# Kernel tuning notes

Measured on AMD Instinct MI355X. Metric: run time of the kernel, lower is better.

Reference implementation:

```python
import jax, jax.numpy as jnp
import numpy as np

B = 4096          # walker batch
S0, S1 = 8, 8     # up / down spins
N = S0 + S1       # total electrons
M = 4             # nucleons
D = 16            # determinants
N_ONE = [256, 256, 256, 256]
N_TWO = [32, 32, 32, 32]


def setup_inputs() -> dict:
    key = jax.random.key(0)
    ks = jax.random.split(key, 16)
    f0 = 8 + 3 * 4 * M              # 56, first-layer one-stream input
    f1 = 3 * N_ONE[0] + 2 * N_TWO[0]  # 832, later-layer one-stream input
    s = 0.05
    return {
        "x": jax.random.normal(ks[0], (B, N, 3), jnp.float32),
        "nucleon_pos": jnp.asarray([[0.0, 0.0, 0.0], [0.0, 0.0, 1.4],
                                    [1.2, 0.0, 0.0], [0.0, 1.2, 0.7]], jnp.float32),
        "v0_w": s * jax.random.normal(ks[1], (N_ONE[0], f0), jnp.float32),
        "v0_b": s * jax.random.normal(ks[2], (N_ONE[0],), jnp.float32),
        "v_w": s * jax.random.normal(ks[3], (3, N_ONE[0], f1), jnp.float32),
        "v_b": s * jax.random.normal(ks[4], (3, N_ONE[0]), jnp.float32),
        "w0_w": s * jax.random.normal(ks[5], (N_TWO[0], 4), jnp.float32),
        "w0_b": s * jax.random.normal(ks[6], (N_TWO[0],), jnp.float32),
        "w_w": s * jax.random.normal(ks[7], (3, N_TWO[0], N_TWO[0]), jnp.float32),
        "w_b": s * jax.random.normal(ks[8], (3, N_TWO[0]), jnp.float32),
        "env_w": s * jax.random.normal(ks[9], (D, N, N_ONE[-1]), jnp.float32),
        "env_g": jax.random.uniform(ks[10], (D, N), jnp.float32),
        "sigma": jax.random.uniform(ks[11], (D, N, M), jnp.float32),
        "pi": jax.random.uniform(ks[12], (D, N, M), jnp.float32),
    }


def _safe_norm(v, axis):
    # ||v||_2 with a zero (not NaN) gradient at v == 0 (diagonal e-e distances).
    s = jnp.sum(v * v, axis=axis)
    return jnp.sqrt(jnp.where(s == 0, 1.0, s)) * (s > 0)


def reference(x, nucleon_pos, v0_w, v0_b, v_w, v_b, w0_w, w0_b, w_w, w_b,
              env_w, env_g, sigma, pi):
    b = x.shape[0]
    # electron-electron stream: [B,N,N,4], [b,i,j] = x_j - x_i, |x_j - x_i|
    tev = x[:, None, :, :] - x[:, :, None, :]
    two = jnp.concatenate([tev, _safe_norm(tev, -1)[..., None]], axis=-1)
    # electron-nucleus: oev[b,m,n] = x_n - R_m  -> [B,M,N,3]
    oev = x[:, None, :, :] - nucleon_pos[:, None, :]
    oed = jnp.linalg.norm(oev, axis=-1)                     # [B,M,N]
    one = jnp.concatenate([oev, oed[..., None]], axis=-1)   # [B,M,N,4]
    one = jnp.transpose(one, (0, 2, 1, 3)).reshape(b, N, 4 * M)  # [B,N,4M]
    oev_p = jnp.transpose(oev, (0, 2, 1, 3))                # [B,N,M,3]

    for l in range(len(N_ONE)):
        g1u = jnp.mean(one[:, :S0], axis=1)                 # [B,F]
        g1d = jnp.mean(one[:, S0:], axis=1)
        g2u = jnp.mean(two[:, :, :S0, :], axis=2)           # [B,N,F2]
        g2d = jnp.mean(two[:, :, S0:, :], axis=2)
        f = jnp.concatenate([
            one,
            jnp.broadcast_to(g1u[:, None], (b, N, g1u.shape[-1])),
            jnp.broadcast_to(g1d[:, None], (b, N, g1d.shape[-1])),
            g2u, g2d], axis=-1)
        Wv, bv = (v0_w, v0_b) if l == 0 else (v_w[l - 1], v_b[l - 1])
        Ww, bw = (w0_w, w0_b) if l == 0 else (w_w[l - 1], w_b[l - 1])
        new_one = jnp.tanh(jnp.einsum('bnf,of->bno', f, Wv) + bv)
        new_two = jnp.tanh(jnp.einsum('bijf,of->bijo', two, Ww) + bw)
        if l > 0 and N_ONE[l] == N_ONE[l - 1] and N_TWO[l] == N_TWO[l - 1]:
            new_one = new_one + one
            new_two = new_two + two
        one, two = new_one, new_two

    r = jnp.linalg.norm(oev_p, axis=-1)                     # [B,N,M]
    F = N_ONE[-1]

    def block(rows, cols):
        ew = env_w[:, rows]                # [D,ni,F]
        eg = env_g[:, rows]                # [D,ni]
        sg = jnp.abs(sigma[:, rows])       # [D,ni,M]
        pw = pi[:, rows]                   # [D,ni,M]
        h = one[:, cols]                   # [B,nj,F]
        rj = r[:, cols]                    # [B,nj,M]
        # sum_f (w*h + g) = w.h + F*g
        lin = jnp.einsum('kif,bjf->bkij', ew, h) + F * eg[None, :, :, None]
        env = jnp.zeros(lin.shape, lin.dtype)
        for m in range(M):                 # small static loop over nucleons
            env = env + pw[None, :, :, None, m] * jnp.exp(
                -sg[None, :, :, None, m] * rj[:, None, None, :, m])
        return lin * env                   # [B,D,ni,nj]

    psi_up = block(slice(0, S0), slice(0, S0))
    psi_dn = block(slice(0, S1), slice(S0, N))  # original reuses row params k*N+i
    d = jnp.linalg.det(psi_up) * jnp.linalg.det(psi_dn)     # [B,D]
    return jnp.sum(d, axis=1)                               # [B]
```

## Files before the change

kernel.cpp:

```cpp
#include <hip/hip_runtime.h>
#include <cmath>

namespace {

typedef unsigned short u16;
typedef unsigned int u32;
using short8  = __attribute__((ext_vector_type(8))) short;
using float4v = __attribute__((ext_vector_type(4))) float;

constexpr size_t MB_HI   = 0;
constexpr size_t MB_LO   = 638976;
constexpr size_t L0_HI   = 1277952;
constexpr size_t L0_LO   = L0_HI + 16384;
constexpr size_t ENV_HI  = L0_LO + 16384;
constexpr size_t ENV_LO  = ENV_HI + 32768;
constexpr size_t TWOB_HI = ENV_LO + 32768;
constexpr size_t TWOB_LO = TWOB_HI + 4096;

__device__ __forceinline__ u16 f2bf(float f) {
    u32 u = __float_as_uint(f);
    u += 0x7FFFu + ((u >> 16) & 1u);
    return (u16)(u >> 16);
}
__device__ __forceinline__ float bf2f(u16 h) {
    return __uint_as_float(((u32)h) << 16);
}
__device__ __forceinline__ float fast_tanh(float x) {
    float e = __expf(-2.f * fabsf(x));
    float t = (1.f - e) * __builtin_amdgcn_rcpf(1.f + e);
    return copysignf(t, x);
}

__global__ void k_prep_main(const float* __restrict__ vw, u16* __restrict__ hi, u16* __restrict__ lo) {
    int id = blockIdx.x * 256 + threadIdx.x;
    int l = id / 212992, rem = id % 212992;
    int ks = rem >> 13;
    int r2 = rem & 8191;
    int nt = r2 >> 9, lane = (r2 >> 3) & 63, j = r2 & 7;
    int n = nt * 16 + (lane & 15);
    int f = ks * 32 + ((lane >> 4) << 3) + j;
    float w = vw[(size_t)(l * 256 + n) * 832 + f];
    u16 h = f2bf(w);
    hi[id] = h; lo[id] = f2bf(w - bf2f(h));
}
__global__ void k_prep_l0(const float* __restrict__ v0w, u16* __restrict__ hi, u16* __restrict__ lo) {
    int id = blockIdx.x * 256 + threadIdx.x;
    int ks = id >> 13;
    int r2 = id & 8191;
    int nt = r2 >> 9, lane = (r2 >> 3) & 63, j = r2 & 7;
    int n = nt * 16 + (lane & 15);
    int f = ks * 32 + ((lane >> 4) << 3) + j;
    float w = (f < 56) ? v0w[n * 56 + f] : 0.f;
    u16 h = f2bf(w);
    hi[id] = h; lo[id] = f2bf(w - bf2f(h));
}
__global__ void k_prep_env(const float* __restrict__ ew, u16* __restrict__ hi, u16* __restrict__ lo) {
    int id = blockIdx.x * 256 + threadIdx.x;
    int ks = id >> 12;
    int r2 = id & 4095;
    int nt = r2 >> 9, lane = (r2 >> 3) & 63, j = r2 & 7;
    int n = nt * 16 + (lane & 15);
    int f = ks * 32 + ((lane >> 4) << 3) + j;
    float w = ew[(size_t)(((n >> 3) * 16) + (n & 7)) * 256 + f];
    u16 h = f2bf(w);
    hi[id] = h; lo[id] = f2bf(w - bf2f(h));
}
__global__ void k_prep_two(const float* __restrict__ w0w, const float* __restrict__ ww,
                           u16* __restrict__ hi, u16* __restrict__ lo) {
    int id = blockIdx.x * 256 + threadIdx.x;
    int l = id >> 10, r = id & 1023;
    int nt = r >> 9, lane = (r >> 3) & 63, j = r & 7;
    int n = nt * 16 + (lane & 15);
    int f = ((lane >> 4) << 3) + j;
    float w;
    if (l == 0) w = (f < 4) ? w0w[n * 4 + f] : 0.f;
    else        w = ww[(size_t)(((l - 1) * 32) + n) * 32 + f];
    u16 h = f2bf(w);
    hi[id] = h; lo[id] = f2bf(w - bf2f(h));
}

template <bool L0, bool RES, bool LAST>
__device__ __forceinline__ void layer_run(
    int t, float (&prev)[4][4], short8 (&twoA)[2][4],
    u16 (*stateF)[32][16][8], u16 (*g2F)[8][16][8], u16 (*g1F)[2][8][4][8],
    float (*twoS)[36],
    const u16* __restrict__ Bhi, const u16* __restrict__ Blo,
    const u16* __restrict__ TBhi, const u16* __restrict__ TBlo,
    const float* __restrict__ bvp, const float* __restrict__ bwp)
{
    const int lane = t & 63, wv = t >> 6, quad = lane >> 4, l16 = lane & 15;
    float4v acc[4];
    #pragma unroll
    for (int q = 0; q < 4; ++q) acc[q] = (float4v){0.f, 0.f, 0.f, 0.f};

    const size_t wb0 = (size_t)(wv * 4) * 512 + (size_t)lane * 8;

    auto mfma_step = [&](int ks, short8 Ah, short8 Al) {
        const u16* bh = Bhi + wb0 + (size_t)ks * 8192;
        const u16* bl = Blo + wb0 + (size_t)ks * 8192;
        #pragma unroll
        for (int q = 0; q < 4; ++q) {
            short8 Wh = *(const short8*)(bh + q * 512);
            short8 Wl = *(const short8*)(bl + q * 512);
            acc[q] = __builtin_amdgcn_mfma_f32_16x16x32_bf16(Ah, Wh, acc[q], 0, 0, 0);
            acc[q] = __builtin_amdgcn_mfma_f32_16x16x32_bf16(Al, Wh, acc[q], 0, 0, 0);
            acc[q] = __builtin_amdgcn_mfma_f32_16x16x32_bf16(Ah, Wl, acc[q], 0, 0, 0);
        }
    };

    if (L0) {
        #pragma unroll
        for (int ks = 0; ks < 2; ++ks) {
            short8 Ah = *(const short8*)&g2F[0][ks * 4 + quad][l16][0];
            short8 Al = *(const short8*)&g2F[1][ks * 4 + quad][l16][0];
            mfma_step(ks, Ah, Al);
        }
    } else {
        #pragma unroll 2
        for (int ks = 0; ks < 8; ++ks) {
            short8 Ah = *(const short8*)&stateF[0][ks * 4 + quad][l16][0];
            short8 Al = *(const short8*)&stateF[1][ks * 4 + quad][l16][0];
            mfma_step(ks, Ah, Al);
        }
        #pragma unroll 2
        for (int ks = 8; ks < 24; ++ks) {
            const int ud = (ks < 16) ? 0 : 1;
            const int kg = (ks - 8) & 7;
            short8 Ah = *(const short8*)&g1F[0][ud][kg][quad][0];
            short8 Al = *(const short8*)&g1F[1][ud][kg][quad][0];
            mfma_step(ks, Ah, Al);
        }
        #pragma unroll
        for (int ks = 24; ks < 26; ++ks) {
            short8 Ah = *(const short8*)&g2F[0][(ks - 24) * 4 + quad][l16][0];
            short8 Al = *(const short8*)&g2F[1][(ks - 24) * 4 + quad][l16][0];
            mfma_step(ks, Ah, Al);
        }
    }
    __syncthreads();

    #pragma unroll
    for (int q = 0; q < 4; ++q) {
        const int n = (wv * 4 + q) * 16 + l16;
        const float bvv = bvp[n];
        #pragma unroll
        for (int r = 0; r < 4; ++r) {
            float v = fast_tanh(acc[q][r] + bvv);
            if (RES) v += prev[q][r];
            prev[q][r] = v;
        }
        if (!LAST) {
            float su = 0.f, sd = 0.f;
            #pragma unroll
            for (int r = 0; r < 4; ++r) { if (quad < 2) su += prev[q][r]; else sd += prev[q][r]; }
            su += __shfl_xor(su, 16); su += __shfl_xor(su, 32);
            sd += __shfl_xor(sd, 16); sd += __shfl_xor(sd, 32);
            if (quad == 0) {
                const int kg = n >> 5, qd = (n >> 3) & 3, jj = n & 7;
                float mu = su * 0.125f, md = sd * 0.125f;
                u16 hu = f2bf(mu), hd = f2bf(md);
                g1F[0][0][kg][qd][jj] = hu; g1F[1][0][kg][qd][jj] = f2bf(mu - bf2f(hu));
                g1F[0][1][kg][qd][jj] = hd; g1F[1][1][kg][qd][jj] = f2bf(md - bf2f(hd));
            }
        }
        const int ko = n >> 3, jj = n & 7;
        #pragma unroll
        for (int r = 0; r < 4; ++r) {
            const int m = quad * 4 + r;
            u16 h = f2bf(prev[q][r]);
            stateF[0][ko][m][jj] = h;
            stateF[1][ko][m][jj] = f2bf(prev[q][r] - bf2f(h));
        }
    }

    if (!LAST) {
        short8 TWh[2], TWl[2];
        #pragma unroll
        for (int nt = 0; nt < 2; ++nt) {
            TWh[nt] = *(const short8*)(TBhi + nt * 512 + (size_t)lane * 8);
            TWl[nt] = *(const short8*)(TBlo + nt * 512 + (size_t)lane * 8);
        }
        #pragma unroll
        for (int mt = 0; mt < 4; ++mt) {
            const int it = wv * 4 + mt;
            float4v tac[2];
            tac[0] = (float4v){0.f, 0.f, 0.f, 0.f};
            tac[1] = (float4v){0.f, 0.f, 0.f, 0.f};
            #pragma unroll
            for (int nt = 0; nt < 2; ++nt) {
                tac[nt] = __builtin_amdgcn_mfma_f32_16x16x32_bf16(twoA[0][mt], TWh[nt], tac[nt], 0, 0, 0);
                tac[nt] = __builtin_amdgcn_mfma_f32_16x16x32_bf16(twoA[1][mt], TWh[nt], tac[nt], 0, 0, 0);
                tac[nt] = __builtin_amdgcn_mfma_f32_16x16x32_bf16(twoA[0][mt], TWl[nt], tac[nt], 0, 0, 0);
            }
            #pragma unroll
            for (int nt = 0; nt < 2; ++nt) {
                const int c = nt * 16 + l16;
                const float bwv = bwp[c];
                #pragma unroll
                for (int r = 0; r < 4; ++r)
                    twoS[quad * 4 + r][c] = fast_tanh(tac[nt][r] + bwv);
            }
            float4 ra = *(const float4*)&twoS[l16][quad * 8];
            float4 rb = *(const float4*)&twoS[l16][quad * 8 + 4];
            float nv[8] = {ra.x, ra.y, ra.z, ra.w, rb.x, rb.y, rb.z, rb.w};
            #pragma unroll
            for (int j2 = 0; j2 < 8; ++j2) {
                float v = nv[j2];
                if (RES) v += bf2f((u16)twoA[0][mt][j2]) + bf2f((u16)twoA[1][mt][j2]);
                nv[j2] = v;
                u16 h = f2bf(v);
                twoA[0][mt][j2] = (short)h;
                twoA[1][mt][j2] = (short)f2bf(v - bf2f(h));
            }
            #pragma unroll
            for (int j2 = 0; j2 < 8; ++j2) {
                float s = nv[j2];
                s += __shfl_xor(s, 1); s += __shfl_xor(s, 2); s += __shfl_xor(s, 4);
                nv[j2] = s * 0.125f;
            }
            if (l16 == 0 || l16 == 8) {
                const int base = (l16 == 0) ? 0 : 4;
                #pragma unroll
                for (int j2 = 0; j2 < 8; ++j2) {
                    u16 h = f2bf(nv[j2]);
                    g2F[0][base + quad][it][j2] = h;
                    g2F[1][base + quad][it][j2] = f2bf(nv[j2] - bf2f(h));
                }
            }
        }
    }
    __syncthreads();
}

__global__ __launch_bounds__(256, 4) void ferminet_kernel(
    const float* __restrict__ x,
    const float* __restrict__ nuc,
    const float* __restrict__ v0_b,
    const float* __restrict__ v_b,
    const float* __restrict__ w0_b,
    const float* __restrict__ w_b,
    const float* __restrict__ env_g,
    const float* __restrict__ sigma,
    const float* __restrict__ pi_,
    const u16* __restrict__ wsB,
    float* __restrict__ out)
{
    __shared__ u16  stateF[2][32][16][8];
    __shared__ u16  g2F[2][8][16][8];
    __shared__ u16  g1F[2][2][8][4][8];
    __shared__ float twoS[4][16][36];
    __shared__ float xs[48];
    __shared__ float rs[64];
    __shared__ float dets[2][16];
    float* psi = (float*)&stateF[0][0][0][0];

    const int t = threadIdx.x;
    const int b = blockIdx.x;
    const int lane = t & 63, wv = t >> 6, quad = lane >> 4, l16 = lane & 15;

    if (t < 48) xs[t] = x[(size_t)b * 48 + t];
    if (t >= 128 && t < 192) ((u32*)&g2F[0][7][0][0])[t - 128] = 0u;
    if (t >= 192 && t < 256) ((u32*)&g2F[1][7][0][0])[t - 192] = 0u;
    __syncthreads();

    if (t < 64) {
        int n = t >> 2, m = t & 3;
        float ox = xs[n * 3 + 0] - nuc[m * 3 + 0];
        float oy = xs[n * 3 + 1] - nuc[m * 3 + 1];
        float oz = xs[n * 3 + 2] - nuc[m * 3 + 2];
        float d = sqrtf(ox * ox + oy * oy + oz * oz);
        rs[n * 4 + m] = d;
        float v[4] = {ox, oy, oz, d};
        #pragma unroll
        for (int c = 0; c < 4; ++c) {
            int k = m * 4 + c;
            u16 h = f2bf(v[c]);
            g2F[0][k >> 3][n][k & 7] = h;
            g2F[1][k >> 3][n][k & 7] = f2bf(v[c] - bf2f(h));
        }
        #pragma unroll
        for (int c = 0; c < 4; ++c) {
            float s = v[c];
            s += __shfl_xor(s, 4); s += __shfl_xor(s, 8); s += __shfl_xor(s, 16);
            if ((n & 7) == 0) {
                float mn = s * 0.125f;
                int k = 16 + (n >> 3) * 16 + m * 4 + c;
                u16 h = f2bf(mn);
                u16 lo = f2bf(mn - bf2f(h));
                #pragma unroll
                for (int mm = 0; mm < 16; ++mm) {
                    g2F[0][k >> 3][mm][k & 7] = h;
                    g2F[1][k >> 3][mm][k & 7] = lo;
                }
            }
        }
    }
    if (t < 128) {
        int i = t >> 3, ud = (t >> 2) & 1, c = t & 3;
        float s = 0.f;
        #pragma unroll
        for (int jo = 0; jo < 8; ++jo) {
            int j = ud * 8 + jo;
            float dx = xs[j * 3 + 0] - xs[i * 3 + 0];
            float dy = xs[j * 3 + 1] - xs[i * 3 + 1];
            float dz = xs[j * 3 + 2] - xs[i * 3 + 2];
            float v;
            if (c == 0) v = dx;
            else if (c == 1) v = dy;
            else if (c == 2) v = dz;
            else { float s2 = dx * dx + dy * dy + dz * dz; v = (s2 > 0.f) ? sqrtf(s2) : 0.f; }
            s += v;
        }
        float mn = s * 0.125f;
        int k = 48 + ud * 4 + c;
        u16 h = f2bf(mn);
        g2F[0][6][i][k & 7] = h;
        g2F[1][6][i][k & 7] = f2bf(mn - bf2f(h));
    }
    short8 twoA[2][4];
    {
        short8 z8 = {0, 0, 0, 0, 0, 0, 0, 0};
        #pragma unroll
        for (int mt = 0; mt < 4; ++mt) { twoA[0][mt] = z8; twoA[1][mt] = z8; }
        if (quad == 0) {
            #pragma unroll
            for (int mt = 0; mt < 4; ++mt) {
                const int it = wv * 4 + mt;
                float dx = xs[l16 * 3 + 0] - xs[it * 3 + 0];
                float dy = xs[l16 * 3 + 1] - xs[it * 3 + 1];
                float dz = xs[l16 * 3 + 2] - xs[it * 3 + 2];
                float s2 = dx * dx + dy * dy + dz * dz;
                float nr = (s2 > 0.f) ? sqrtf(s2) : 0.f;
                float v[4] = {dx, dy, dz, nr};
                #pragma unroll
                for (int c = 0; c < 4; ++c) {
                    u16 h = f2bf(v[c]);
                    twoA[0][mt][c] = (short)h;
                    twoA[1][mt][c] = (short)f2bf(v[c] - bf2f(h));
                }
            }
        }
    }
    __syncthreads();

    float prev[4][4];
    layer_run<true,  false, false>(t, prev, twoA, stateF, g2F, g1F, twoS[wv],
        wsB + L0_HI, wsB + L0_LO, wsB + TWOB_HI, wsB + TWOB_LO, v0_b, w0_b);
    layer_run<false, true,  false>(t, prev, twoA, stateF, g2F, g1F, twoS[wv],
        wsB + MB_HI + 0 * 212992, wsB + MB_LO + 0 * 212992,
        wsB + TWOB_HI + 1024, wsB + TWOB_LO + 1024, v_b + 0 * 256, w_b + 0 * 32);
    layer_run<false, true,  false>(t, prev, twoA, stateF, g2F, g1F, twoS[wv],
        wsB + MB_HI + 1 * 212992, wsB + MB_LO + 1 * 212992,
        wsB + TWOB_HI + 2048, wsB + TWOB_LO + 2048, v_b + 1 * 256, w_b + 1 * 32);
    layer_run<false, true,  true >(t, prev, twoA, stateF, g2F, g1F, twoS[wv],
        wsB + MB_HI + 2 * 212992, wsB + MB_LO + 2 * 212992,
        wsB + TWOB_HI + 3072, wsB + TWOB_LO + 3072, v_b + 2 * 256, w_b + 2 * 32);

    {
        float4v ac2[2];
        ac2[0] = (float4v){0.f, 0.f, 0.f, 0.f};
        ac2[1] = (float4v){0.f, 0.f, 0.f, 0.f};
        const size_t wb0 = (size_t)(wv * 2) * 512 + (size_t)lane * 8;
        const u16* Eh = wsB + ENV_HI;
        const u16* El = wsB + ENV_LO;
        #pragma unroll 2
        for (int ks = 0; ks < 8; ++ks) {
            short8 Ah = *(const short8*)&stateF[0][ks * 4 + quad][l16][0];
            short8 Al = *(const short8*)&stateF[1][ks * 4 + quad][l16][0];
            const u16* bh = Eh + wb0 + (size_t)ks * 4096;
            const u16* bl = El + wb0 + (size_t)ks * 4096;
            #pragma unroll
            for (int q = 0; q < 2; ++q) {
                short8 Wh = *(const short8*)(bh + q * 512);
                short8 Wl = *(const short8*)(bl + q * 512);
                ac2[q] = __builtin_amdgcn_mfma_f32_16x16x32_bf16(Ah, Wh, ac2[q], 0, 0, 0);
                ac2[q] = __builtin_amdgcn_mfma_f32_16x16x32_bf16(Al, Wh, ac2[q], 0, 0, 0);
                ac2[q] = __builtin_amdgcn_mfma_f32_16x16x32_bf16(Ah, Wl, ac2[q], 0, 0, 0);
            }
        }
        float vals[2][4];
        int kk[2], ii[2];
        #pragma unroll
        for (int q = 0; q < 2; ++q) {
            const int n = (wv * 2 + q) * 16 + l16;
            const int k = n >> 3, i = n & 7, kif = k * 16 + i;
            kk[q] = k; ii[q] = i;
            const float lc = 256.f * env_g[kif];
            const float4 pw4 = *(const float4*)&pi_[(size_t)kif * 4];
            const float4 sg4 = *(const float4*)&sigma[(size_t)kif * 4];
            const float sg[4] = {fabsf(sg4.x), fabsf(sg4.y), fabsf(sg4.z), fabsf(sg4.w)};
            const float pw[4] = {pw4.x, pw4.y, pw4.z, pw4.w};
            #pragma unroll
            for (int r = 0; r < 4; ++r) {
                const int je = quad * 4 + r;
                float E = 0.f;
                #pragma unroll
                for (int m = 0; m < 4; ++m) E += pw[m] * __expf(-sg[m] * rs[je * 4 + m]);
                vals[q][r] = (ac2[q][r] + lc) * E;
            }
        }
        __syncthreads();
        #pragma unroll
        for (int q = 0; q < 2; ++q) {
            #pragma unroll
            for (int r = 0; r < 4; ++r) {
                const int je = quad * 4 + r;
                const int s = je >> 3, j = je & 7;
                psi[((s * 16 + kk[q]) * 8 + ii[q]) * 8 + j] = vals[q][r];
            }
        }
    }
    __syncthreads();

    if (t < 32) {
        int s = t >> 4, k = t & 15;
        const float* src = psi + (s * 16 + k) * 64;
        float m[8][8];
        #pragma unroll
        for (int i = 0; i < 8; ++i)
            #pragma unroll
            for (int j = 0; j < 8; ++j) m[i][j] = src[i * 8 + j];
        float det = 1.f;
        #pragma unroll
        for (int c = 0; c < 8; ++c) {
            #pragma unroll
            for (int r = c + 1; r < 8; ++r) {
                if (fabsf(m[r][c]) > fabsf(m[c][c])) {
                    det = -det;
                    #pragma unroll
                    for (int j = 0; j < 8; ++j) {
                        float tmp = m[c][j]; m[c][j] = m[r][j]; m[r][j] = tmp;
                    }
                }
            }
            float piv = m[c][c];
            det *= piv;
            if (piv != 0.f) {
                float inv = 1.f / piv;
                #pragma unroll
                for (int r = c + 1; r < 8; ++r) {
                    float fac = m[r][c] * inv;
                    #pragma unroll
                    for (int j = c; j < 8; ++j) m[r][j] -= fac * m[c][j];
                }
            }
        }
        dets[s][k] = det;
    }
    __syncthreads();

    if (t == 0) {
        float s = 0.f;
        #pragma unroll
        for (int k = 0; k < 16; ++k) s += dets[0][k] * dets[1][k];
        out[b] = s;
    }
}

}

extern "C" void kernel_launch(void* const* d_in, const int* in_sizes, int n_in,
                              void* d_out, int out_size, void* d_ws, size_t ws_size,
                              hipStream_t stream) {
    (void)n_in; (void)out_size; (void)ws_size;
    const float* x    = (const float*)d_in[0];
    const float* nuc  = (const float*)d_in[1];
    const float* v0w  = (const float*)d_in[2];
    const float* v0b  = (const float*)d_in[3];
    const float* vw   = (const float*)d_in[4];
    const float* vb   = (const float*)d_in[5];
    const float* w0w  = (const float*)d_in[6];
    const float* w0b  = (const float*)d_in[7];
    const float* ww   = (const float*)d_in[8];
    const float* wb   = (const float*)d_in[9];
    const float* envw = (const float*)d_in[10];
    const float* envg = (const float*)d_in[11];
    const float* sig  = (const float*)d_in[12];
    const float* pii  = (const float*)d_in[13];
    float* out = (float*)d_out;
    u16* wsB = (u16*)d_ws;

    k_prep_main<<<638976 / 256, 256, 0, stream>>>(vw, wsB + MB_HI, wsB + MB_LO);
    k_prep_l0  <<<16384 / 256, 256, 0, stream>>>(v0w, wsB + L0_HI, wsB + L0_LO);
    k_prep_env <<<32768 / 256, 256, 0, stream>>>(envw, wsB + ENV_HI, wsB + ENV_LO);
    k_prep_two <<<4096 / 256, 256, 0, stream>>>(w0w, ww, wsB + TWOB_HI, wsB + TWOB_LO);

    const int B = in_sizes[0] / 48;
    ferminet_kernel<<<B, 256, 0, stream>>>(x, nuc, v0b, vb, w0b, wb,
                                           envg, sig, pii, wsB, out);
}
```

Baseline: 575.5 us.

## Process two walkers per 512-thread block with duplicated shared state

Each block now runs 512 threads and handles two walkers, with shared-memory buffers duplicated per walker half and a walker index derived from the thread id. The aim is to halve the block count and let the two walkers' waves share cached weight loads and overlap each other's latency within one workgroup. In exchange, shared memory per block doubles, every __syncthreads now stalls both walkers together, and the launch bounds of 512x4 may squeeze registers. An odd batch size would leave the last walker unprocessed.

```diff
diff --git a/kernel.cpp b/kernel.cpp
--- a/kernel.cpp
+++ b/kernel.cpp
@@ -81,14 +81,14 @@
 
 template <bool L0, bool RES, bool LAST>
 __device__ __forceinline__ void layer_run(
-    int t, float (&prev)[4][4], short8 (&twoA)[2][4],
+    int lane, int wv, float (&prev)[4][4], short8 (&twoA)[2][4],
     u16 (*stateF)[32][16][8], u16 (*g2F)[8][16][8], u16 (*g1F)[2][8][4][8],
     float (*twoS)[36],
     const u16* __restrict__ Bhi, const u16* __restrict__ Blo,
     const u16* __restrict__ TBhi, const u16* __restrict__ TBlo,
     const float* __restrict__ bvp, const float* __restrict__ bwp)
 {
-    const int lane = t & 63, wv = t >> 6, quad = lane >> 4, l16 = lane & 15;
+    const int quad = lane >> 4, l16 = lane & 15;
     float4v acc[4];
     #pragma unroll
     for (int q = 0; q < 4; ++q) acc[q] = (float4v){0.f, 0.f, 0.f, 0.f};
@@ -232,7 +232,7 @@
     __syncthreads();
 }
 
-__global__ __launch_bounds__(256, 4) void ferminet_kernel(
+__global__ __launch_bounds__(512, 4) void ferminet_kernel(
     const float* __restrict__ x,
     const float* __restrict__ nuc,
     const float* __restrict__ v0_b,
@@ -245,38 +245,43 @@
     const u16* __restrict__ wsB,
     float* __restrict__ out)
 {
-    __shared__ u16  stateF[2][32][16][8];
-    __shared__ u16  g2F[2][8][16][8];
-    __shared__ u16  g1F[2][2][8][4][8];
-    __shared__ float twoS[4][16][36];
-    __shared__ float xs[48];
-    __shared__ float rs[64];
-    __shared__ float dets[2][16];
-    float* psi = (float*)&stateF[0][0][0][0];
+    __shared__ u16  stateF[2][2][32][16][8];
+    __shared__ u16  g2F[2][2][8][16][8];
+    __shared__ u16  g1F[2][2][2][8][4][8];
+    __shared__ float twoS[8][16][36];
+    __shared__ float xs[2][48];
+    __shared__ float rs[2][64];
+    __shared__ float dets[2][2][16];
 
     const int t = threadIdx.x;
     const int b = blockIdx.x;
-    const int lane = t & 63, wv = t >> 6, quad = lane >> 4, l16 = lane & 15;
-
-    if (t < 48) xs[t] = x[(size_t)b * 48 + t];
-    if (t >= 128 && t < 192) ((u32*)&g2F[0][7][0][0])[t - 128] = 0u;
-    if (t >= 192 && t < 256) ((u32*)&g2F[1][7][0][0])[t - 192] = 0u;
-    __syncthreads();
-
-    if (t < 64) {
-        int n = t >> 2, m = t & 3;
-        float ox = xs[n * 3 + 0] - nuc[m * 3 + 0];
-        float oy = xs[n * 3 + 1] - nuc[m * 3 + 1];
-        float oz = xs[n * 3 + 2] - nuc[m * 3 + 2];
+    const int wk = t >> 8;
+    const int tw = t & 255;
+    const int lane = t & 63;
+    const int wv = (t >> 6) & 3;
+    const int gw = t >> 6;
+    const int quad = lane >> 4, l16 = lane & 15;
+    float* psi = (float*)&stateF[wk][0][0][0][0];
+
+    if (tw < 48) xs[wk][tw] = x[((size_t)b * 2 + wk) * 48 + tw];
+    if (tw >= 128 && tw < 192) ((u32*)&g2F[wk][0][7][0][0])[tw - 128] = 0u;
+    if (tw >= 192)             ((u32*)&g2F[wk][1][7][0][0])[tw - 192] = 0u;
+    __syncthreads();
+
+    if (tw < 64) {
+        int n = tw >> 2, m = tw & 3;
+        float ox = xs[wk][n * 3 + 0] - nuc[m * 3 + 0];
+        float oy = xs[wk][n * 3 + 1] - nuc[m * 3 + 1];
+        float oz = xs[wk][n * 3 + 2] - nuc[m * 3 + 2];
         float d = sqrtf(ox * ox + oy * oy + oz * oz);
-        rs[n * 4 + m] = d;
+        rs[wk][n * 4 + m] = d;
         float v[4] = {ox, oy, oz, d};
         #pragma unroll
         for (int c = 0; c < 4; ++c) {
             int k = m * 4 + c;
             u16 h = f2bf(v[c]);
-            g2F[0][k >> 3][n][k & 7] = h;
-            g2F[1][k >> 3][n][k & 7] = f2bf(v[c] - bf2f(h));
+            g2F[wk][0][k >> 3][n][k & 7] = h;
+            g2F[wk][1][k >> 3][n][k & 7] = f2bf(v[c] - bf2f(h));
         }
         #pragma unroll
         for (int c = 0; c < 4; ++c) {
@@ -289,21 +294,21 @@
                 u16 lo = f2bf(mn - bf2f(h));
                 #pragma unroll
                 for (int mm = 0; mm < 16; ++mm) {
-                    g2F[0][k >> 3][mm][k & 7] = h;
-                    g2F[1][k >> 3][mm][k & 7] = lo;
+                    g2F[wk][0][k >> 3][mm][k & 7] = h;
+                    g2F[wk][1][k >> 3][mm][k & 7] = lo;
                 }
             }
         }
     }
-    if (t < 128) {
-        int i = t >> 3, ud = (t >> 2) & 1, c = t & 3;
+    if (tw < 128) {
+        int i = tw >> 3, ud = (tw >> 2) & 1, c = tw & 3;
         float s = 0.f;
         #pragma unroll
         for (int jo = 0; jo < 8; ++jo) {
             int j = ud * 8 + jo;
-            float dx = xs[j * 3 + 0] - xs[i * 3 + 0];
-            float dy = xs[j * 3 + 1] - xs[i * 3 + 1];
-            float dz = xs[j * 3 + 2] - xs[i * 3 + 2];
+            float dx = xs[wk][j * 3 + 0] - xs[wk][i * 3 + 0];
+            float dy = xs[wk][j * 3 + 1] - xs[wk][i * 3 + 1];
+            float dz = xs[wk][j * 3 + 2] - xs[wk][i * 3 + 2];
             float v;
             if (c == 0) v = dx;
             else if (c == 1) v = dy;
@@ -314,8 +319,8 @@
         float mn = s * 0.125f;
         int k = 48 + ud * 4 + c;
         u16 h = f2bf(mn);
-        g2F[0][6][i][k & 7] = h;
-        g2F[1][6][i][k & 7] = f2bf(mn - bf2f(h));
+        g2F[wk][0][6][i][k & 7] = h;
+        g2F[wk][1][6][i][k & 7] = f2bf(mn - bf2f(h));
     }
     short8 twoA[2][4];
     {
@@ -326,9 +331,9 @@
             #pragma unroll
             for (int mt = 0; mt < 4; ++mt) {
                 const int it = wv * 4 + mt;
-                float dx = xs[l16 * 3 + 0] - xs[it * 3 + 0];
-                float dy = xs[l16 * 3 + 1] - xs[it * 3 + 1];
-                float dz = xs[l16 * 3 + 2] - xs[it * 3 + 2];
+                float dx = xs[wk][l16 * 3 + 0] - xs[wk][it * 3 + 0];
+                float dy = xs[wk][l16 * 3 + 1] - xs[wk][it * 3 + 1];
+                float dz = xs[wk][l16 * 3 + 2] - xs[wk][it * 3 + 2];
                 float s2 = dx * dx + dy * dy + dz * dz;
                 float nr = (s2 > 0.f) ? sqrtf(s2) : 0.f;
                 float v[4] = {dx, dy, dz, nr};
@@ -344,15 +349,15 @@
     __syncthreads();
 
     float prev[4][4];
-    layer_run<true,  false, false>(t, prev, twoA, stateF, g2F, g1F, twoS[wv],
+    layer_run<true,  false, false>(lane, wv, prev, twoA, stateF[wk], g2F[wk], g1F[wk], twoS[gw],
         wsB + L0_HI, wsB + L0_LO, wsB + TWOB_HI, wsB + TWOB_LO, v0_b, w0_b);
-    layer_run<false, true,  false>(t, prev, twoA, stateF, g2F, g1F, twoS[wv],
+    layer_run<false, true,  false>(lane, wv, prev, twoA, stateF[wk], g2F[wk], g1F[wk], twoS[gw],
         wsB + MB_HI + 0 * 212992, wsB + MB_LO + 0 * 212992,
         wsB + TWOB_HI + 1024, wsB + TWOB_LO + 1024, v_b + 0 * 256, w_b + 0 * 32);
-    layer_run<false, true,  false>(t, prev, twoA, stateF, g2F, g1F, twoS[wv],
+    layer_run<false, true,  false>(lane, wv, prev, twoA, stateF[wk], g2F[wk], g1F[wk], twoS[gw],
         wsB + MB_HI + 1 * 212992, wsB + MB_LO + 1 * 212992,
         wsB + TWOB_HI + 2048, wsB + TWOB_LO + 2048, v_b + 1 * 256, w_b + 1 * 32);
-    layer_run<false, true,  true >(t, prev, twoA, stateF, g2F, g1F, twoS[wv],
+    layer_run<false, true,  true >(lane, wv, prev, twoA, stateF[wk], g2F[wk], g1F[wk], twoS[gw],
         wsB + MB_HI + 2 * 212992, wsB + MB_LO + 2 * 212992,
         wsB + TWOB_HI + 3072, wsB + TWOB_LO + 3072, v_b + 2 * 256, w_b + 2 * 32);
 
@@ -365,8 +370,8 @@
         const u16* El = wsB + ENV_LO;
         #pragma unroll 2
         for (int ks = 0; ks < 8; ++ks) {
-            short8 Ah = *(const short8*)&stateF[0][ks * 4 + quad][l16][0];
-            short8 Al = *(const short8*)&stateF[1][ks * 4 + quad][l16][0];
+            short8 Ah = *(const short8*)&stateF[wk][0][ks * 4 + quad][l16][0];
+            short8 Al = *(const short8*)&stateF[wk][1][ks * 4 + quad][l16][0];
             const u16* bh = Eh + wb0 + (size_t)ks * 4096;
             const u16* bl = El + wb0 + (size_t)ks * 4096;
             #pragma unroll
@@ -395,7 +400,7 @@
                 const int je = quad * 4 + r;
                 float E = 0.f;
                 #pragma unroll
-                for (int m = 0; m < 4; ++m) E += pw[m] * __expf(-sg[m] * rs[je * 4 + m]);
+                for (int m = 0; m < 4; ++m) E += pw[m] * __expf(-sg[m] * rs[wk][je * 4 + m]);
                 vals[q][r] = (ac2[q][r] + lc) * E;
             }
         }
@@ -412,8 +417,8 @@
     }
     __syncthreads();
 
-    if (t < 32) {
-        int s = t >> 4, k = t & 15;
+    if (tw < 32) {
+        int s = tw >> 4, k = tw & 15;
         const float* src = psi + (s * 16 + k) * 64;
         float m[8][8];
         #pragma unroll
@@ -445,15 +450,15 @@
                 }
             }
         }
-        dets[s][k] = det;
-    }
-    __syncthreads();
-
-    if (t == 0) {
+        dets[wk][s][k] = det;
+    }
+    __syncthreads();
+
+    if (tw == 0) {
         float s = 0.f;
         #pragma unroll
-        for (int k = 0; k < 16; ++k) s += dets[0][k] * dets[1][k];
-        out[b] = s;
+        for (int k = 0; k < 16; ++k) s += dets[wk][0][k] * dets[wk][1][k];
+        out[(size_t)b * 2 + wk] = s;
     }
 }
 
@@ -486,6 +491,6 @@
     k_prep_two <<<4096 / 256, 256, 0, stream>>>(w0w, ww, wsB + TWOB_HI, wsB + TWOB_LO);
 
     const int B = in_sizes[0] / 48;
-    ferminet_kernel<<<B, 256, 0, stream>>>(x, nuc, v0b, vb, w0b, wb,
-                                           envg, sig, pii, wsB, out);
-}
+    ferminet_kernel<<<B / 2, 512, 0, stream>>>(x, nuc, v0b, vb, w0b, wb,
+                                               envg, sig, pii, wsB, out);
+}
```

New measurement: 605.5 us. +5.2%, slower.
